# Performance work log

Measured on AMD Instinct MI355X. Metric: run time of the kernel, lower is better.

## Reference

```python
import jax, jax.numpy as jnp
import numpy as np

# Dims matching init_kwargs
B, S, D = 2, 2048, 1024
H, E, P, K = 8, 8, 128, 2
SCALE = 1.0 / np.sqrt(P)  # registered buffer 'scale'


def setup_inputs() -> dict:
    key = jax.random.key(0)
    ks = jax.random.split(key, 8)
    std = 1.0 / np.sqrt(D)  # reset_parameters uses std_scale/sqrt(input_size)
    return {
        "x": jax.random.normal(ks[0], (B, S, D), jnp.float32),
        "q_w": jax.random.normal(ks[1], (H * P, D), jnp.float32) * std,
        "k_w": jax.random.normal(ks[2], (H * P, D), jnp.float32) * std,
        "v_w": jax.random.normal(ks[3], (H * E, D, P), jnp.float32) * std,
        "o_w": jax.random.normal(ks[4], (H * E, P, D), jnp.float32) * (1.0 / np.sqrt(H * P)),
        "sel_v_w": jax.random.normal(ks[5], (H * E, D), jnp.float32) * std,
        "sel_o_w": jax.random.normal(ks[6], (H * E, D), jnp.float32) * std,
        "route_scale": jnp.ones((1,), jnp.float32),
    }


def _get_sel_gate(x, w, route_scale):
    """Faithful port of SwitchHeadCore.get_sel (eval mode, no bias):
    sigmoid routing logits per head, top-k expert selection, weight
    normalization, route_scale. Returned as a dense [B,S,H,E] gate so the
    indexed expert combine is expressed as a gated einsum (same math)."""
    logits = jnp.einsum('bsd,ed->bse', x, w).astype(jnp.float32)
    raw = logits.reshape(x.shape[0], x.shape[1], H, E)
    probs = jax.nn.sigmoid(raw)
    vals, idx = jax.lax.top_k(probs, K)                 # [B,S,H,K]
    vals = vals / jnp.clip(vals.sum(-1, keepdims=True), 1e-9)  # normalize_weights
    vals = vals * route_scale
    gate = (jax.nn.one_hot(idx, E, dtype=vals.dtype) * vals[..., None]).sum(-2)
    return gate  # [B,S,H,E]


def reference(x, q_w, k_w, v_w, o_w, sel_v_w, sel_o_w, route_scale):
    rs = route_scale[0]
    gate_v = _get_sel_gate(x, sel_v_w, rs)  # [B,S,H,E]
    gate_o = _get_sel_gate(x, sel_o_w, rs)  # [B,S,H,E]

    # q/k projections -> torch head order [B,H,S,P]
    q = jnp.einsum('bsd,hpd->bhsp', x, q_w.reshape(H, P, D))
    k = jnp.einsum('bsd,hpd->bhsp', x, k_w.reshape(H, P, D))

    # Per-token expert V projection: mixture of selected expert weight slices
    xv = jnp.einsum('bsd,hedp->bshep', x, v_w.reshape(H, E, D, P))
    v = jnp.einsum('bshep,bshe->bhsp', xv, gate_v)

    # Scaled dot-product attention (eval: no dropout)
    att = jax.nn.softmax(jnp.einsum('bhqp,bhkp->bhqk', q, k) * SCALE, axis=-1)
    ctx = jnp.einsum('bhqk,bhkp->bqhp', att, v)  # [B,S,H,P]

    # Per-token expert O projection, gated, summed over heads
    weighted = ctx[:, :, :, None, :] * gate_o[..., None]  # [B,S,H,E,P]
    out = jnp.einsum('bshep,hepd->bsd', weighted, o_w.reshape(H, E, P, D))
    return out
```

## Files before the change

### kernel.cpp

```cpp
#include <hip/hip_runtime.h>


typedef unsigned short u16;
typedef __attribute__((ext_vector_type(8))) short s8v;
typedef __attribute__((ext_vector_type(4))) float f4v;
typedef __attribute__((ext_vector_type(4))) unsigned short us4;

#define ATT_SCALE 0.08838834764831845f

__device__ inline u16 bf16_rne(float f) {
  union { float f; unsigned u; } v; v.f = f;
  unsigned r = v.u + 0x7fffu + ((v.u >> 16) & 1u);
  return (u16)(r >> 16);
}
__device__ inline float bf2f(u16 h) {
  union { unsigned u; float f; } v; v.u = ((unsigned)h) << 16;
  return v.f;
}

__device__ inline void glds16(const void* g, void* l) {
  __builtin_amdgcn_global_load_lds((const __attribute__((address_space(1))) void*)g,
                                   (__attribute__((address_space(3))) void*)l, 16, 0, 0);
}
__device__ inline int swzcol(int idx) {
  int r = idx >> 2;
  return (((idx & 3) ^ ((r + (r >> 2)) & 3)) << 3);
}
#define WAITB() do { asm volatile("s_waitcnt vmcnt(0)" ::: "memory"); __syncthreads(); } while (0)

__global__ void conv_qk(const float* __restrict__ Q, const float* __restrict__ K,
                        u16* __restrict__ Qb, u16* __restrict__ Kb) {
  int i = blockIdx.x * 256 + threadIdx.x;
  const float* src; u16* dst; int off;
  if (i < 262144) { src = Q; dst = Qb; off = i; }
  else            { src = K; dst = Kb; off = i - 262144; }
  float4 v = *(const float4*)&src[(size_t)off * 4];
  us4 o; o[0]=bf16_rne(v.x); o[1]=bf16_rne(v.y); o[2]=bf16_rne(v.z); o[3]=bf16_rne(v.w);
  *(us4*)&dst[(size_t)off * 4] = o;
}

__global__ void transpose_w(const float* __restrict__ src, u16* __restrict__ dst, int mode) {
  __shared__ float tile[32][33];
  int he = blockIdx.z;
  int C = mode ? 1024 : 128;
  int r0 = blockIdx.y * 32, c0 = blockIdx.x * 32;
  int lc = threadIdx.x & 31, rr = threadIdx.x >> 5;
  const float* s = src + (size_t)he * 131072;
#pragma unroll
  for (int i = 0; i < 4; ++i) {
    int r = rr + i * 8;
    tile[r][lc] = s[(size_t)(r0 + r) * C + c0 + lc];
  }
  __syncthreads();
#pragma unroll
  for (int i = 0; i < 4; ++i) {
    int c = rr + i * 8;
    float v = tile[lc][c];
    size_t a;
    if (mode) a = (size_t)(c0 + c) * 8192 + (size_t)he * 128 + (r0 + lc);
    else      a = (size_t)(he >> 3) * 1048576 + (size_t)(c0 + c) * 8192 + (size_t)(he & 7) * 1024 + (r0 + lc);
    dst[a] = bf16_rne(v);
  }
}

__global__ __launch_bounds__(256, 2) void routing(
    const float* __restrict__ X, const float* __restrict__ SelV, const float* __restrict__ SelO,
    const float* __restrict__ RS, int2* __restrict__ Tvi, float2* __restrict__ Tvg,
    int2* __restrict__ Toi, float2* __restrict__ Tog, u16* __restrict__ Xb) {
  __shared__ float xs[8][1024];
  __shared__ float lgs[8][128];
  int t0 = blockIdx.x * 8;
  int tid = threadIdx.x;
  for (int i = tid; i < 2048; i += 256) {
    int row = i >> 8, c = (i & 255) * 4;
    float4 v = *(const float4*)&X[(size_t)(t0 + row) * 1024 + c];
    *(float4*)&xs[row][c] = v;
    us4 o; o[0]=bf16_rne(v.x); o[1]=bf16_rne(v.y); o[2]=bf16_rne(v.z); o[3]=bf16_rne(v.w);
    *(us4*)&Xb[(size_t)(t0 + row) * 1024 + c] = o;
  }
  __syncthreads();
  {
    int widx = tid & 127, tg = tid >> 7;
    const float* w = (widx < 64) ? (SelV + (size_t)widx * 1024) : (SelO + (size_t)(widx - 64) * 1024);
    float acc[4] = {0.f, 0.f, 0.f, 0.f};
    for (int k = 0; k < 1024; k += 4) {
      float4 wv = *(const float4*)&w[k];
#pragma unroll
      for (int t = 0; t < 4; ++t) {
        float4 xv = *(const float4*)&xs[tg * 4 + t][k];
        acc[t] += wv.x * xv.x + wv.y * xv.y + wv.z * xv.z + wv.w * xv.w;
      }
    }
#pragma unroll
    for (int t = 0; t < 4; ++t) lgs[tg * 4 + t][widx] = acc[t];
  }
  __syncthreads();
  if (tid < 128) {
    float rs = RS[0];
    int tok = tid >> 4, which = (tid >> 3) & 1, h = tid & 7;
    float p[8];
#pragma unroll
    for (int e = 0; e < 8; ++e)
      p[e] = 1.f / (1.f + __expf(-lgs[tok][which * 64 + h * 8 + e]));
    float v1 = -1.f; int i1 = -1;
#pragma unroll
    for (int e = 0; e < 8; ++e) if (p[e] > v1) { v1 = p[e]; i1 = e; }
    float v2 = -1.f; int i2 = -1;
#pragma unroll
    for (int e = 0; e < 8; ++e) if (e != i1 && p[e] > v2) { v2 = p[e]; i2 = e; }
    float ssum = fmaxf(v1 + v2, 1e-9f);
    float g1 = v1 / ssum * rs, g2 = v2 / ssum * rs;
    int t = t0 + tok;
    int lo, hi; float glo, ghi;
    if (i1 < i2) { lo = i1; hi = i2; glo = g1; ghi = g2; }
    else         { lo = i2; hi = i1; glo = g2; ghi = g1; }
    if (which) { Toi[t * 8 + h] = make_int2(lo, hi); Tog[t * 8 + h] = make_float2(glo, ghi); }
    else       { Tvi[t * 8 + h] = make_int2(lo, hi); Tvg[t * 8 + h] = make_float2(glo, ghi); }
  }
}

__global__ __launch_bounds__(256) void build_buckets2(
    const int2* __restrict__ Tvi, const float2* __restrict__ Tvg,
    int* __restrict__ bcnt, u16* __restrict__ btok, float* __restrict__ bgate) {
  const int h = blockIdx.x;
  const int tid = threadIdx.x;
  const int lane = tid & 63;
  __shared__ int cnt[8];
  if (tid < 8) cnt[tid] = 0;
  __syncthreads();
  for (int chunk = 0; chunk < 16; ++chunk) {
    int t = chunk * 256 + tid;
    int2 e = Tvi[t * 8 + h];
    float2 g = Tvg[t * 8 + h];
#pragma unroll
    for (int role = 0; role < 2; ++role) {
      int mye = role ? e.y : e.x;
      float myg = role ? g.y : g.x;
      u16 entry = role ? (u16)(t | 0x8000) : (u16)t;
#pragma unroll
      for (int ee = 0; ee < 8; ++ee) {
        unsigned long long mask = __ballot(mye == ee);
        if (mye == ee) {
          int prefix = __popcll(mask & ((1ull << lane) - 1ull));
          int leader = __ffsll((unsigned long long)mask) - 1;
          int base = 0;
          if (lane == leader) base = atomicAdd(&cnt[ee], (int)__popcll(mask));
          base = __shfl(base, leader);
          int pos = base + prefix;
          btok[(h * 8 + ee) * 4096 + pos] = entry;
          bgate[(h * 8 + ee) * 4096 + pos] = myg;
        }
      }
    }
  }
  __syncthreads();
  if (tid < 8) bcnt[h * 8 + tid] = cnt[tid];
}

__global__ __launch_bounds__(256) void gemm_qk(
    const u16* __restrict__ Xb, const u16* __restrict__ Wq, const u16* __restrict__ Wk,
    u16* __restrict__ Qo, u16* __restrict__ Ko) {
  __shared__ u16 Ash0[64 * 32], Ash1[64 * 32];
  __shared__ u16 Bsh0[128 * 32], Bsh1[128 * 32];
  const int tb = blockIdx.x, nb = blockIdx.y;
  const u16* W = blockIdx.z ? Wk : Wq;
  u16* Out = blockIdx.z ? Ko : Qo;
  const int tid = threadIdx.x;
  const int wave = tid >> 6, lane = tid & 63;
  const int lg = lane >> 4, lr = lane & 15;
  const int r0 = tid >> 2, r1 = (tid + 256) >> 2;
  const int c0 = swzcol(tid), c1 = swzcol(tid + 256);
  const size_t aw  = (size_t)(tb * 64 + r0) * 1024 + c0;
  const size_t bw0 = (size_t)(nb * 128 + r0) * 1024 + c0;
  const size_t bw1 = (size_t)(nb * 128 + r1) * 1024 + c1;
  const int csl = (lg ^ ((lr + (lr >> 2)) & 3)) << 3;
  f4v acc[4][2] = {};
#define STG_QK(A, B, k0) do { \
    glds16(&Xb[aw + (k0)], &A[tid * 8]); \
    glds16(&W[bw0 + (k0)], &B[tid * 8]); \
    glds16(&W[bw1 + (k0)], &B[(tid + 256) * 8]); \
  } while (0)
#define CMP_QK(A, B) do { \
    s8v af[4], bfr[2]; \
    _Pragma("unroll") for (int m = 0; m < 4; ++m) af[m] = *(const s8v*)&A[(m * 16 + lr) * 32 + csl]; \
    _Pragma("unroll") for (int n = 0; n < 2; ++n) bfr[n] = *(const s8v*)&B[(wave * 32 + n * 16 + lr) * 32 + csl]; \
    _Pragma("unroll") for (int m = 0; m < 4; ++m) \
      _Pragma("unroll") for (int n = 0; n < 2; ++n) \
        acc[m][n] = __builtin_amdgcn_mfma_f32_16x16x32_bf16(af[m], bfr[n], acc[m][n], 0, 0, 0); \
  } while (0)
  STG_QK(Ash0, Bsh0, 0);
  for (int kt = 0; kt < 32; kt += 2) {
    WAITB();
    if (kt + 1 < 32) STG_QK(Ash1, Bsh1, (kt + 1) * 32);
    CMP_QK(Ash0, Bsh0);
    WAITB();
    if (kt + 2 < 32) STG_QK(Ash0, Bsh0, (kt + 2) * 32);
    CMP_QK(Ash1, Bsh1);
  }
#undef STG_QK
#undef CMP_QK
#pragma unroll
  for (int m = 0; m < 4; ++m) {
    int tbase = tb * 64 + m * 16 + lg * 4;
    int b = tbase >> 11, s = tbase & 2047;
#pragma unroll
    for (int n = 0; n < 2; ++n) {
      int p = wave * 32 + n * 16 + lr;
      size_t base = ((size_t)(b * 8 + nb) * 2048 + s) * 128 + p;
#pragma unroll
      for (int j = 0; j < 4; ++j)
        Out[base + (size_t)j * 128] = bf16_rne(acc[m][n][j]);
    }
  }
}

__global__ __launch_bounds__(256) void gemm_v_e(
    const u16* __restrict__ Xb, const u16* __restrict__ Vw ,
    const int* __restrict__ bcnt, const u16* __restrict__ btok,
    const float* __restrict__ bgate, u16* __restrict__ VpA, u16* __restrict__ VpB) {
  const int id = blockIdx.x + 32 * blockIdx.y;
  const int xk = id & 7, j = id >> 3;
  const int bucket = 8 * xk + (j & 7);
  const int tile = j >> 3;
  const int h = bucket >> 3, e = bucket & 7;
  const int cnt = bcnt[bucket];
  if (tile * 128 >= cnt) return;
  __shared__ u16 Ash0[128 * 32], Ash1[128 * 32];
  __shared__ u16 Bsh0[128 * 32], Bsh1[128 * 32];
  __shared__ int toksh[128];
  __shared__ float gsh[128];
  const int tid = threadIdx.x;
  if (tid < 128) {
    int ar = tile * 128 + tid;
    if (ar < cnt) {
      toksh[tid] = btok[bucket * 4096 + ar];
      gsh[tid] = bgate[bucket * 4096 + ar];
    } else { toksh[tid] = 0; gsh[tid] = 0.f; }
  }
  __syncthreads();
  const int wave = tid >> 6, lane = tid & 63;
  const int wm = wave >> 1, wn = wave & 1;
  const int lg = lane >> 4, lr = lane & 15;
  const int r0 = tid >> 2, r1 = (tid + 256) >> 2;
  const int c0 = swzcol(tid), c1 = swzcol(tid + 256);
  const size_t aw0 = (size_t)(toksh[r0] & 0xFFF) * 1024 + c0;
  const size_t aw1 = (size_t)(toksh[r1] & 0xFFF) * 1024 + c1;
  const size_t bw0 = ((size_t)(h * 128 + r0) * 8 + e) * 1024 + c0;
  const size_t bw1 = ((size_t)(h * 128 + r1) * 8 + e) * 1024 + c1;
  const int csl = (lg ^ ((lr + (lr >> 2)) & 3)) << 3;
  f4v acc[4][4] = {};
#define STG_VE(A, B, k0) do { \
    glds16(&Xb[aw0 + (k0)], &A[tid * 8]); \
    glds16(&Xb[aw1 + (k0)], &A[(tid + 256) * 8]); \
    glds16(&Vw[bw0 + (k0)], &B[tid * 8]); \
    glds16(&Vw[bw1 + (k0)], &B[(tid + 256) * 8]); \
  } while (0)
#define CMP_VE(A, B) do { \
    s8v af[4], bfr[4]; \
    _Pragma("unroll") for (int m = 0; m < 4; ++m) af[m] = *(const s8v*)&A[(wm * 64 + m * 16 + lr) * 32 + csl]; \
    _Pragma("unroll") for (int n = 0; n < 4; ++n) bfr[n] = *(const s8v*)&B[(wn * 64 + n * 16 + lr) * 32 + csl]; \
    _Pragma("unroll") for (int m = 0; m < 4; ++m) \
      _Pragma("unroll") for (int n = 0; n < 4; ++n) \
        acc[m][n] = __builtin_amdgcn_mfma_f32_16x16x32_bf16(af[m], bfr[n], acc[m][n], 0, 0, 0); \
  } while (0)
  STG_VE(Ash0, Bsh0, 0);
  for (int kt = 0; kt < 32; kt += 2) {
    WAITB();
    if (kt + 1 < 32) STG_VE(Ash1, Bsh1, (kt + 1) * 32);
    CMP_VE(Ash0, Bsh0);
    WAITB();
    if (kt + 2 < 32) STG_VE(Ash0, Bsh0, (kt + 2) * 32);
    CMP_VE(Ash1, Bsh1);
  }
#undef STG_VE
#undef CMP_VE
#pragma unroll
  for (int m = 0; m < 4; ++m) {
#pragma unroll
    for (int j2 = 0; j2 < 4; ++j2) {
      int row = wm * 64 + m * 16 + lg * 4 + j2;
      int ar = tile * 128 + row;
      if (ar < cnt) {
        int entry = toksh[row];
        int tok = entry & 0xFFF;
        u16* dst = (entry & 0x8000) ? VpB : VpA;
        float g = gsh[row];
#pragma unroll
        for (int n = 0; n < 4; ++n) {
          int p = wn * 64 + n * 16 + lr;
          dst[(size_t)tok * 1024 + h * 128 + p] = bf16_rne(g * acc[m][n][j2]);
        }
      }
    }
  }
}

__global__ void vadd_transpose(const u16* __restrict__ VpA, const u16* __restrict__ VpB,
                               u16* __restrict__ VT) {
  __shared__ u16 tile[64][136];
  const int sb = blockIdx.x, bh = blockIdx.y;
  const int b = bh >> 3, h = bh & 7;
  const int tid = threadIdx.x;
#pragma unroll
  for (int it = 0; it < 4; ++it) {
    int idx = tid + it * 256;
    int r = idx >> 4, c8 = (idx & 15) << 3;
    size_t off = (size_t)(b * 2048 + sb * 64 + r) * 1024 + h * 128 + c8;
    s8v va = *(const s8v*)&VpA[off];
    s8v vb = *(const s8v*)&VpB[off];
    s8v o;
#pragma unroll
    for (int j = 0; j < 8; ++j) o[j] = (short)bf16_rne(bf2f((u16)va[j]) + bf2f((u16)vb[j]));
    *(s8v*)&tile[r][c8] = o;
  }
  __syncthreads();
#pragma unroll
  for (int it = 0; it < 8; ++it) {
    int idx = tid + it * 256;
    int p = idx >> 4, c4 = (idx & 15) << 2;
    us4 o;
#pragma unroll
    for (int j = 0; j < 4; ++j) o[j] = tile[c4 + j][p];
    *(us4*)&VT[((size_t)bh * 128 + p) * 2048 + sb * 64 + c4] = o;
  }
}

__global__ __launch_bounds__(256, 2) void attn(
    const u16* __restrict__ Q, const u16* __restrict__ K,
    const u16* __restrict__ VT, u16* __restrict__ CTX) {
  __shared__ u16 Kt[64 * 136];
  __shared__ u16 Vt[128 * 72];
  __shared__ u16 Pl[4][16 * 72];
  const int id = blockIdx.x + 32 * blockIdx.y;
  const int xk = id & 7, j = id >> 3;
  const int bh = 2 * xk + (j >> 5);
  const int qb = j & 31;
  const int tid = threadIdx.x;
  const int wave = tid >> 6, lane = tid & 63;
  const int lg = lane >> 4, lr = lane & 15;
  const size_t base = (size_t)bh * 2048 * 128;
  const int q0 = qb * 64 + wave * 16;
  s8v qf[4];
#pragma unroll
  for (int ks = 0; ks < 4; ++ks)
    qf[ks] = *(const s8v*)&Q[base + (size_t)(q0 + lr) * 128 + ks * 32 + lg * 8];
  s8v kr[4], vr[4];
#define LOADKV(kb) do { \
    _Pragma("unroll") for (int i = 0; i < 4; ++i) { \
      int idx = tid + i * 256; \
      kr[i] = *(const s8v*)&K[base + (size_t)((kb) * 64 + (idx >> 4)) * 128 + ((idx & 15) << 3)]; \
      vr[i] = *(const s8v*)&VT[base + (size_t)(idx >> 3) * 2048 + (kb) * 64 + ((idx & 7) << 3)]; \
    } } while (0)
#define WRITEKV() do { \
    _Pragma("unroll") for (int i = 0; i < 4; ++i) { \
      int idx = tid + i * 256; \
      *(s8v*)&Kt[(idx >> 4) * 136 + ((idx & 15) << 3)] = kr[i]; \
      *(s8v*)&Vt[(idx >> 3) * 72 + ((idx & 7) << 3)] = vr[i]; \
    } } while (0)
  f4v cacc[8] = {};
  float mrun = -1e30f, ssum = 0.f;
  LOADKV(0);
  for (int kb = 0; kb < 32; ++kb) {
    asm volatile("s_waitcnt vmcnt(0)" ::: "memory");
    __syncthreads();
    WRITEKV();
    __syncthreads();
    if (kb + 1 < 32) LOADKV(kb + 1);
    f4v sc[4] = {};
    __builtin_amdgcn_s_setprio(1);
#pragma unroll
    for (int ks = 0; ks < 4; ++ks) {
#pragma unroll
      for (int m = 0; m < 4; ++m) {
        s8v ak = *(const s8v*)&Kt[(m * 16 + lr) * 136 + ks * 32 + lg * 8];
        sc[m] = __builtin_amdgcn_mfma_f32_16x16x32_bf16(ak, qf[ks], sc[m], 0, 0, 0);
      }
    }
    __builtin_amdgcn_s_setprio(0);
    float tmax = -1e30f;
#pragma unroll
    for (int m = 0; m < 4; ++m)
#pragma unroll
      for (int j2 = 0; j2 < 4; ++j2) {
        float v = sc[m][j2] * ATT_SCALE;
        sc[m][j2] = v;
        tmax = fmaxf(tmax, v);
      }
    tmax = fmaxf(tmax, __shfl_xor(tmax, 16));
    tmax = fmaxf(tmax, __shfl_xor(tmax, 32));
    float mnew = fmaxf(mrun, tmax);
    float f = __expf(mrun - mnew);
    mrun = mnew;
    float psum = 0.f;
#pragma unroll
    for (int m = 0; m < 4; ++m) {
      us4 pk;
#pragma unroll
      for (int j2 = 0; j2 < 4; ++j2) {
        float pe = __expf(sc[m][j2] - mnew);
        psum += pe;
        pk[j2] = bf16_rne(pe);
      }
      *(us4*)&Pl[wave][lr * 72 + m * 16 + lg * 4] = pk;
    }
    psum += __shfl_xor(psum, 16);
    psum += __shfl_xor(psum, 32);
    ssum = ssum * f + psum;
#pragma unroll
    for (int mr = 0; mr < 8; ++mr)
#pragma unroll
      for (int j2 = 0; j2 < 4; ++j2) cacc[mr][j2] *= f;
    __builtin_amdgcn_s_setprio(1);
#pragma unroll
    for (int ks = 0; ks < 2; ++ks) {
      s8v bp = *(const s8v*)&Pl[wave][lr * 72 + ks * 32 + lg * 8];
#pragma unroll
      for (int mr = 0; mr < 8; ++mr) {
        s8v av = *(const s8v*)&Vt[(mr * 16 + lr) * 72 + ks * 32 + lg * 8];
        cacc[mr] = __builtin_amdgcn_mfma_f32_16x16x32_bf16(av, bp, cacc[mr], 0, 0, 0);
      }
    }
    __builtin_amdgcn_s_setprio(0);
  }
#undef LOADKV
#undef WRITEKV
  float rinv = 1.f / ssum;
#pragma unroll
  for (int mr = 0; mr < 8; ++mr) {
    us4 pk;
#pragma unroll
    for (int j2 = 0; j2 < 4; ++j2) pk[j2] = bf16_rne(cacc[mr][j2] * rinv);
    *(us4*)&CTX[base + (size_t)(q0 + lr) * 128 + mr * 16 + lg * 4] = pk;
  }
}

__global__ __launch_bounds__(256) void pregate(
    const u16* __restrict__ CTX, const int2* __restrict__ Toi, const float2* __restrict__ Tog,
    u16* __restrict__ CTXG) {
  const int t = blockIdx.x;
  const int tid = threadIdx.x;
  __shared__ float gsh[64];
  if (tid < 64) {
    int h = tid >> 3, e = tid & 7;
    int2 ei = Toi[t * 8 + h];
    float2 gg = Tog[t * 8 + h];
    gsh[tid] = (e == ei.x) ? gg.x : ((e == ei.y) ? gg.y : 0.f);
  }
  __syncthreads();
  const int b = t >> 11, s = t & 2047;
#pragma unroll
  for (int c = 0; c < 4; ++c) {
    int chunk = tid + c * 256;
    int he = chunk >> 4, p8 = (chunk & 15) << 3;
    int h = he >> 3;
    float g = gsh[he];
    s8v o;
    if (g != 0.f) {
      s8v v = *(const s8v*)&CTX[((size_t)(b * 8 + h) * 2048 + s) * 128 + p8];
#pragma unroll
      for (int j = 0; j < 8; ++j) o[j] = (short)bf16_rne(bf2f((u16)v[j]) * g);
    } else {
#pragma unroll
      for (int j = 0; j < 8; ++j) o[j] = 0;
    }
    *(s8v*)&CTXG[(size_t)t * 8192 + chunk * 8] = o;
  }
}

__global__ __launch_bounds__(256) void gemm_o_dense(
    const u16* __restrict__ CTXG, const u16* __restrict__ Ow ,
    float* __restrict__ OUT, float* __restrict__ OP1a, float* __restrict__ OP1b) {
  __shared__ u16 Ash0[128 * 32], Ash1[128 * 32];
  __shared__ u16 Bsh0[128 * 32], Bsh1[128 * 32];
  const int tb = blockIdx.x, db = blockIdx.y, kz = blockIdx.z;
  const int tid = threadIdx.x;
  const int wave = tid >> 6, lane = tid & 63;
  const int wm = wave >> 1, wn = wave & 1;
  const int lg = lane >> 4, lr = lane & 15;
  const size_t kbase = (size_t)kz * 4096;
  const int r0 = tid >> 2, r1 = (tid + 256) >> 2;
  const int c0 = swzcol(tid), c1 = swzcol(tid + 256);
  const size_t aw0 = (size_t)(tb * 128 + r0) * 8192 + kbase + c0;
  const size_t aw1 = (size_t)(tb * 128 + r1) * 8192 + kbase + c1;
  const size_t bw0 = (size_t)(db * 128 + r0) * 8192 + kbase + c0;
  const size_t bw1 = (size_t)(db * 128 + r1) * 8192 + kbase + c1;
  const int csl = (lg ^ ((lr + (lr >> 2)) & 3)) << 3;
  f4v acc[4][4] = {};
#define STG_O(A, B, k0) do { \
    glds16(&CTXG[aw0 + (k0)], &A[tid * 8]); \
    glds16(&CTXG[aw1 + (k0)], &A[(tid + 256) * 8]); \
    glds16(&Ow[bw0 + (k0)], &B[tid * 8]); \
    glds16(&Ow[bw1 + (k0)], &B[(tid + 256) * 8]); \
  } while (0)
#define CMP_O(A, B) do { \
    s8v af[4], bfr[4]; \
    _Pragma("unroll") for (int m = 0; m < 4; ++m) af[m] = *(const s8v*)&A[(wm * 64 + m * 16 + lr) * 32 + csl]; \
    _Pragma("unroll") for (int n = 0; n < 4; ++n) bfr[n] = *(const s8v*)&B[(wn * 64 + n * 16 + lr) * 32 + csl]; \
    _Pragma("unroll") for (int m = 0; m < 4; ++m) \
      _Pragma("unroll") for (int n = 0; n < 4; ++n) \
        acc[m][n] = __builtin_amdgcn_mfma_f32_16x16x32_bf16(af[m], bfr[n], acc[m][n], 0, 0, 0); \
  } while (0)
  STG_O(Ash0, Bsh0, 0);
  for (int kt = 0; kt < 128; kt += 2) {
    WAITB();
    if (kt + 1 < 128) STG_O(Ash1, Bsh1, (kt + 1) * 32);
    CMP_O(Ash0, Bsh0);
    WAITB();
    if (kt + 2 < 128) STG_O(Ash0, Bsh0, (kt + 2) * 32);
    CMP_O(Ash1, Bsh1);
  }
#undef STG_O
#undef CMP_O
  float* OP;
  if (kz == 0) OP = OUT;
  else OP = (tb < 16) ? OP1a : OP1b;
  const int toff = (kz == 0) ? tb * 128 : (tb & 15) * 128;
#pragma unroll
  for (int m = 0; m < 4; ++m) {
    int t = toff + wm * 64 + m * 16 + lg * 4;
#pragma unroll
    for (int n = 0; n < 4; ++n) {
      int d = db * 128 + wn * 64 + n * 16 + lr;
#pragma unroll
      for (int j2 = 0; j2 < 4; ++j2)
        OP[(size_t)(t + j2) * 1024 + d] = acc[m][n][j2];
    }
  }
}

__global__ void add_inplace(float* __restrict__ OUT, const float* __restrict__ P0,
                            const float* __restrict__ P1) {
  size_t i = ((size_t)blockIdx.x * 256 + threadIdx.x) * 4;
  const float* P = (i < 2097152) ? (P0 + i) : (P1 + (i - 2097152));
  float4 a = *(const float4*)&OUT[i];
  float4 b = *(const float4*)P;
  *(float4*)&OUT[i] = make_float4(a.x + b.x, a.y + b.y, a.z + b.z, a.w + b.w);
}

extern "C" void kernel_launch(void* const* d_in, const int* in_sizes, int n_in,
                              void* d_out, int out_size, void* d_ws, size_t ws_size,
                              hipStream_t stream) {
  const float* x     = (const float*)d_in[0];
  const float* q_w   = (const float*)d_in[1];
  const float* k_w   = (const float*)d_in[2];
  const float* v_w   = (const float*)d_in[3];
  const float* o_w   = (const float*)d_in[4];
  const float* sel_v = (const float*)d_in[5];
  const float* sel_o = (const float*)d_in[6];
  const float* rs    = (const float*)d_in[7];

  char* ws = (char*)d_ws;
  const size_t MB = 1048576;
  const size_t KB = 1024;
  u16*    xb    = (u16*)(ws);
  u16*    ctx   = (u16*)(ws);
  float*  op1a  = (float*)(ws);
  u16*    qwb   = (u16*)(ws + 8 * MB);
  u16*    kwb   = (u16*)(ws + 10 * MB);
  u16*    ctxg  = (u16*)(ws + 8 * MB);
  u16*    vwT   = (u16*)(ws + 12 * MB);
  u16*    vt    = (u16*)(ws + 12 * MB);
  u16*    vpA   = (u16*)(ws + 28 * MB);
  u16*    vpB   = (u16*)(ws + 36 * MB);
  u16*    qh    = (u16*)(ws + 49 * MB + 512 * KB);
  u16*    kh    = (u16*)(ws + 57 * MB + 512 * KB);
  int2*   tvi   = (int2*)(ws + 72 * MB);
  float2* tvg   = (float2*)(ws + 72 * MB + 256 * KB);
  int2*   toi   = (int2*)(ws + 72 * MB + 512 * KB);
  float2* tog   = (float2*)(ws + 72 * MB + 768 * KB);
  int*    bcnt2 = (int*)(ws + 73 * MB);
  u16*    btok2 = (u16*)(ws + 73 * MB + 4 * KB);
  float*  bgate2= (float*)(ws + 73 * MB + 520 * KB);
  float*  op1b  = (float*)(ws + 72 * MB);
  u16*    owT   = (u16*)(ws + 80 * MB);
  float*  outp  = (float*)d_out;

  hipLaunchKernelGGL(conv_qk, dim3(2048), dim3(256), 0, stream, q_w, k_w, qwb, kwb);
  hipLaunchKernelGGL(transpose_w, dim3(4, 32, 64), dim3(256), 0, stream, v_w, vwT, 0);
  hipLaunchKernelGGL(transpose_w, dim3(32, 4, 64), dim3(256), 0, stream, o_w, owT, 1);
  hipLaunchKernelGGL(routing, dim3(512), dim3(256), 0, stream, x, sel_v, sel_o, rs, tvi, tvg, toi, tog, xb);
  hipLaunchKernelGGL(build_buckets2, dim3(8), dim3(256), 0, stream, tvi, tvg, bcnt2, btok2, bgate2);
  hipLaunchKernelGGL(gemm_v_e, dim3(32, 64), dim3(256), 0, stream, xb, vwT, bcnt2, btok2, bgate2, vpA, vpB);
  hipLaunchKernelGGL(vadd_transpose, dim3(32, 16), dim3(256), 0, stream, vpA, vpB, vt);
  hipLaunchKernelGGL(gemm_qk, dim3(64, 8, 2), dim3(256), 0, stream, xb, qwb, kwb, qh, kh);
  hipLaunchKernelGGL(attn, dim3(32, 16), dim3(256), 0, stream, qh, kh, vt, ctx);
  hipLaunchKernelGGL(pregate, dim3(4096), dim3(256), 0, stream, ctx, toi, tog, ctxg);
  hipLaunchKernelGGL(gemm_o_dense, dim3(32, 8, 2), dim3(256), 0, stream, ctxg, owT, outp, op1a, op1b);
  hipLaunchKernelGGL(add_inplace, dim3(4096), dim3(256), 0, stream, outp, op1a, op1b);
}
```

Measured before the change: 367.5 us.

## Merge prep kernels into one launch and fuse V-expert and QK GEMMs

Folds the weight conversion, the two weight transposes and routing into a single prep_all kernel that branches on block index. It also folds the QK projection GEMM into the expert V GEMM launch, adding 1024 extra blocks. This removes several kernel launches and the gaps between them, and lets the dense QK work fill CUs left idle by sparse expert tiles that exit early. The cost is a larger shared-memory footprint for the merged kernels, which may lower occupancy for the lighter branches.

```diff
diff --git a/kernel.cpp b/kernel.cpp
--- a/kernel.cpp
+++ b/kernel.cpp
@@ -28,94 +28,101 @@
 }
 #define WAITB() do { asm volatile("s_waitcnt vmcnt(0)" ::: "memory"); __syncthreads(); } while (0)
 
-__global__ void conv_qk(const float* __restrict__ Q, const float* __restrict__ K,
-                        u16* __restrict__ Qb, u16* __restrict__ Kb) {
-  int i = blockIdx.x * 256 + threadIdx.x;
-  const float* src; u16* dst; int off;
-  if (i < 262144) { src = Q; dst = Qb; off = i; }
-  else            { src = K; dst = Kb; off = i - 262144; }
-  float4 v = *(const float4*)&src[(size_t)off * 4];
-  us4 o; o[0]=bf16_rne(v.x); o[1]=bf16_rne(v.y); o[2]=bf16_rne(v.z); o[3]=bf16_rne(v.w);
-  *(us4*)&dst[(size_t)off * 4] = o;
-}
-
-__global__ void transpose_w(const float* __restrict__ src, u16* __restrict__ dst, int mode) {
-  __shared__ float tile[32][33];
-  int he = blockIdx.z;
-  int C = mode ? 1024 : 128;
-  int r0 = blockIdx.y * 32, c0 = blockIdx.x * 32;
-  int lc = threadIdx.x & 31, rr = threadIdx.x >> 5;
-  const float* s = src + (size_t)he * 131072;
-#pragma unroll
-  for (int i = 0; i < 4; ++i) {
-    int r = rr + i * 8;
-    tile[r][lc] = s[(size_t)(r0 + r) * C + c0 + lc];
-  }
-  __syncthreads();
-#pragma unroll
-  for (int i = 0; i < 4; ++i) {
-    int c = rr + i * 8;
-    float v = tile[lc][c];
-    size_t a;
-    if (mode) a = (size_t)(c0 + c) * 8192 + (size_t)he * 128 + (r0 + lc);
-    else      a = (size_t)(he >> 3) * 1048576 + (size_t)(c0 + c) * 8192 + (size_t)(he & 7) * 1024 + (r0 + lc);
-    dst[a] = bf16_rne(v);
-  }
-}
-
-__global__ __launch_bounds__(256, 2) void routing(
+__global__ __launch_bounds__(256, 2) void prep_all(
+    const float* __restrict__ Qw, const float* __restrict__ Kw,
+    const float* __restrict__ Vw, const float* __restrict__ Ow,
     const float* __restrict__ X, const float* __restrict__ SelV, const float* __restrict__ SelO,
-    const float* __restrict__ RS, int2* __restrict__ Tvi, float2* __restrict__ Tvg,
+    const float* __restrict__ RS,
+    u16* __restrict__ Qb, u16* __restrict__ Kb, u16* __restrict__ vwT, u16* __restrict__ owT,
+    int2* __restrict__ Tvi, float2* __restrict__ Tvg,
     int2* __restrict__ Toi, float2* __restrict__ Tog, u16* __restrict__ Xb) {
-  __shared__ float xs[8][1024];
-  __shared__ float lgs[8][128];
-  int t0 = blockIdx.x * 8;
-  int tid = threadIdx.x;
-  for (int i = tid; i < 2048; i += 256) {
-    int row = i >> 8, c = (i & 255) * 4;
-    float4 v = *(const float4*)&X[(size_t)(t0 + row) * 1024 + c];
-    *(float4*)&xs[row][c] = v;
+  __shared__ __align__(16) char smem[36864];
+  const int id = blockIdx.x;
+  const int tid = threadIdx.x;
+  if (id < 2048) {
+    int i = id * 256 + tid;
+    const float* src; u16* dst; int off;
+    if (i < 262144) { src = Qw; dst = Qb; off = i; }
+    else            { src = Kw; dst = Kb; off = i - 262144; }
+    float4 v = *(const float4*)&src[(size_t)off * 4];
     us4 o; o[0]=bf16_rne(v.x); o[1]=bf16_rne(v.y); o[2]=bf16_rne(v.z); o[3]=bf16_rne(v.w);
-    *(us4*)&Xb[(size_t)(t0 + row) * 1024 + c] = o;
-  }
-  __syncthreads();
-  {
-    int widx = tid & 127, tg = tid >> 7;
-    const float* w = (widx < 64) ? (SelV + (size_t)widx * 1024) : (SelO + (size_t)(widx - 64) * 1024);
-    float acc[4] = {0.f, 0.f, 0.f, 0.f};
-    for (int k = 0; k < 1024; k += 4) {
-      float4 wv = *(const float4*)&w[k];
-#pragma unroll
-      for (int t = 0; t < 4; ++t) {
-        float4 xv = *(const float4*)&xs[tg * 4 + t][k];
-        acc[t] += wv.x * xv.x + wv.y * xv.y + wv.z * xv.z + wv.w * xv.w;
-      }
-    }
-#pragma unroll
-    for (int t = 0; t < 4; ++t) lgs[tg * 4 + t][widx] = acc[t];
-  }
-  __syncthreads();
-  if (tid < 128) {
-    float rs = RS[0];
-    int tok = tid >> 4, which = (tid >> 3) & 1, h = tid & 7;
-    float p[8];
-#pragma unroll
-    for (int e = 0; e < 8; ++e)
-      p[e] = 1.f / (1.f + __expf(-lgs[tok][which * 64 + h * 8 + e]));
-    float v1 = -1.f; int i1 = -1;
-#pragma unroll
-    for (int e = 0; e < 8; ++e) if (p[e] > v1) { v1 = p[e]; i1 = e; }
-    float v2 = -1.f; int i2 = -1;
-#pragma unroll
-    for (int e = 0; e < 8; ++e) if (e != i1 && p[e] > v2) { v2 = p[e]; i2 = e; }
-    float ssum = fmaxf(v1 + v2, 1e-9f);
-    float g1 = v1 / ssum * rs, g2 = v2 / ssum * rs;
-    int t = t0 + tok;
-    int lo, hi; float glo, ghi;
-    if (i1 < i2) { lo = i1; hi = i2; glo = g1; ghi = g2; }
-    else         { lo = i2; hi = i1; glo = g2; ghi = g1; }
-    if (which) { Toi[t * 8 + h] = make_int2(lo, hi); Tog[t * 8 + h] = make_float2(glo, ghi); }
-    else       { Tvi[t * 8 + h] = make_int2(lo, hi); Tvg[t * 8 + h] = make_float2(glo, ghi); }
+    *(us4*)&dst[(size_t)off * 4] = o;
+  } else if (id < 18432) {
+    float* tile = (float*)smem;
+    int mode, bx, by, he;
+    if (id < 10240) { int rel = id - 2048;  mode = 0; bx = rel & 3;  by = (rel >> 2) & 31; he = rel >> 7; }
+    else            { int rel = id - 10240; mode = 1; bx = rel & 31; by = (rel >> 5) & 3;  he = rel >> 7; }
+    const float* src = mode ? Ow : Vw;
+    u16* dst = mode ? owT : vwT;
+    int C = mode ? 1024 : 128;
+    int r0 = by * 32, c0 = bx * 32;
+    int lc = tid & 31, rr = tid >> 5;
+    const float* s = src + (size_t)he * 131072;
+#pragma unroll
+    for (int i = 0; i < 4; ++i) {
+      int r = rr + i * 8;
+      tile[r * 33 + lc] = s[(size_t)(r0 + r) * C + c0 + lc];
+    }
+    __syncthreads();
+#pragma unroll
+    for (int i = 0; i < 4; ++i) {
+      int c = rr + i * 8;
+      float v = tile[lc * 33 + c];
+      size_t a;
+      if (mode) a = (size_t)(c0 + c) * 8192 + (size_t)he * 128 + (r0 + lc);
+      else      a = (size_t)(he >> 3) * 1048576 + (size_t)(c0 + c) * 8192 + (size_t)(he & 7) * 1024 + (r0 + lc);
+      dst[a] = bf16_rne(v);
+    }
+  } else {
+    float* xs  = (float*)smem;
+    float* lgs = (float*)(smem + 32768);
+    int t0 = (id - 18432) * 8;
+    for (int i = tid; i < 2048; i += 256) {
+      int row = i >> 8, c = (i & 255) * 4;
+      float4 v = *(const float4*)&X[(size_t)(t0 + row) * 1024 + c];
+      *(float4*)&xs[row * 1024 + c] = v;
+      us4 o; o[0]=bf16_rne(v.x); o[1]=bf16_rne(v.y); o[2]=bf16_rne(v.z); o[3]=bf16_rne(v.w);
+      *(us4*)&Xb[(size_t)(t0 + row) * 1024 + c] = o;
+    }
+    __syncthreads();
+    {
+      int widx = tid & 127, tg = tid >> 7;
+      const float* w = (widx < 64) ? (SelV + (size_t)widx * 1024) : (SelO + (size_t)(widx - 64) * 1024);
+      float acc[4] = {0.f, 0.f, 0.f, 0.f};
+      for (int k = 0; k < 1024; k += 4) {
+        float4 wv = *(const float4*)&w[k];
+#pragma unroll
+        for (int t = 0; t < 4; ++t) {
+          float4 xv = *(const float4*)&xs[(tg * 4 + t) * 1024 + k];
+          acc[t] += wv.x * xv.x + wv.y * xv.y + wv.z * xv.z + wv.w * xv.w;
+        }
+      }
+#pragma unroll
+      for (int t = 0; t < 4; ++t) lgs[(tg * 4 + t) * 128 + widx] = acc[t];
+    }
+    __syncthreads();
+    if (tid < 128) {
+      float rs = RS[0];
+      int tok = tid >> 4, which = (tid >> 3) & 1, h = tid & 7;
+      float p[8];
+#pragma unroll
+      for (int e = 0; e < 8; ++e)
+        p[e] = 1.f / (1.f + __expf(-lgs[tok * 128 + which * 64 + h * 8 + e]));
+      float v1 = -1.f; int i1 = -1;
+#pragma unroll
+      for (int e = 0; e < 8; ++e) if (p[e] > v1) { v1 = p[e]; i1 = e; }
+      float v2 = -1.f; int i2 = -1;
+#pragma unroll
+      for (int e = 0; e < 8; ++e) if (e != i1 && p[e] > v2) { v2 = p[e]; i2 = e; }
+      float ssum = fmaxf(v1 + v2, 1e-9f);
+      float g1 = v1 / ssum * rs, g2 = v2 / ssum * rs;
+      int t = t0 + tok;
+      int lo, hi; float glo, ghi;
+      if (i1 < i2) { lo = i1; hi = i2; glo = g1; ghi = g2; }
+      else         { lo = i2; hi = i1; glo = g2; ghi = g1; }
+      if (which) { Toi[t * 8 + h] = make_int2(lo, hi); Tog[t * 8 + h] = make_float2(glo, ghi); }
+      else       { Tvi[t * 8 + h] = make_int2(lo, hi); Tvg[t * 8 + h] = make_float2(glo, ghi); }
+    }
   }
 }
 
@@ -157,98 +164,44 @@
   if (tid < 8) bcnt[h * 8 + tid] = cnt[tid];
 }
 
-__global__ __launch_bounds__(256) void gemm_qk(
-    const u16* __restrict__ Xb, const u16* __restrict__ Wq, const u16* __restrict__ Wk,
+__global__ __launch_bounds__(256) void gemm_v_qk(
+    const u16* __restrict__ Xb, const u16* __restrict__ Vw,
+    const int* __restrict__ bcnt, const u16* __restrict__ btok,
+    const float* __restrict__ bgate, u16* __restrict__ VpA, u16* __restrict__ VpB,
+    const u16* __restrict__ Wq, const u16* __restrict__ Wk,
     u16* __restrict__ Qo, u16* __restrict__ Ko) {
-  __shared__ u16 Ash0[64 * 32], Ash1[64 * 32];
+  __shared__ u16 Ash0[128 * 32], Ash1[128 * 32];
   __shared__ u16 Bsh0[128 * 32], Bsh1[128 * 32];
-  const int tb = blockIdx.x, nb = blockIdx.y;
-  const u16* W = blockIdx.z ? Wk : Wq;
-  u16* Out = blockIdx.z ? Ko : Qo;
+  __shared__ int toksh[128];
+  __shared__ float gsh[128];
   const int tid = threadIdx.x;
   const int wave = tid >> 6, lane = tid & 63;
   const int lg = lane >> 4, lr = lane & 15;
   const int r0 = tid >> 2, r1 = (tid + 256) >> 2;
   const int c0 = swzcol(tid), c1 = swzcol(tid + 256);
-  const size_t aw  = (size_t)(tb * 64 + r0) * 1024 + c0;
-  const size_t bw0 = (size_t)(nb * 128 + r0) * 1024 + c0;
-  const size_t bw1 = (size_t)(nb * 128 + r1) * 1024 + c1;
   const int csl = (lg ^ ((lr + (lr >> 2)) & 3)) << 3;
-  f4v acc[4][2] = {};
-#define STG_QK(A, B, k0) do { \
-    glds16(&Xb[aw + (k0)], &A[tid * 8]); \
-    glds16(&W[bw0 + (k0)], &B[tid * 8]); \
-    glds16(&W[bw1 + (k0)], &B[(tid + 256) * 8]); \
-  } while (0)
-#define CMP_QK(A, B) do { \
-    s8v af[4], bfr[2]; \
-    _Pragma("unroll") for (int m = 0; m < 4; ++m) af[m] = *(const s8v*)&A[(m * 16 + lr) * 32 + csl]; \
-    _Pragma("unroll") for (int n = 0; n < 2; ++n) bfr[n] = *(const s8v*)&B[(wave * 32 + n * 16 + lr) * 32 + csl]; \
-    _Pragma("unroll") for (int m = 0; m < 4; ++m) \
-      _Pragma("unroll") for (int n = 0; n < 2; ++n) \
-        acc[m][n] = __builtin_amdgcn_mfma_f32_16x16x32_bf16(af[m], bfr[n], acc[m][n], 0, 0, 0); \
-  } while (0)
-  STG_QK(Ash0, Bsh0, 0);
-  for (int kt = 0; kt < 32; kt += 2) {
-    WAITB();
-    if (kt + 1 < 32) STG_QK(Ash1, Bsh1, (kt + 1) * 32);
-    CMP_QK(Ash0, Bsh0);
-    WAITB();
-    if (kt + 2 < 32) STG_QK(Ash0, Bsh0, (kt + 2) * 32);
-    CMP_QK(Ash1, Bsh1);
-  }
-#undef STG_QK
-#undef CMP_QK
-#pragma unroll
-  for (int m = 0; m < 4; ++m) {
-    int tbase = tb * 64 + m * 16 + lg * 4;
-    int b = tbase >> 11, s = tbase & 2047;
-#pragma unroll
-    for (int n = 0; n < 2; ++n) {
-      int p = wave * 32 + n * 16 + lr;
-      size_t base = ((size_t)(b * 8 + nb) * 2048 + s) * 128 + p;
-#pragma unroll
-      for (int j = 0; j < 4; ++j)
-        Out[base + (size_t)j * 128] = bf16_rne(acc[m][n][j]);
-    }
-  }
-}
-
-__global__ __launch_bounds__(256) void gemm_v_e(
-    const u16* __restrict__ Xb, const u16* __restrict__ Vw ,
-    const int* __restrict__ bcnt, const u16* __restrict__ btok,
-    const float* __restrict__ bgate, u16* __restrict__ VpA, u16* __restrict__ VpB) {
-  const int id = blockIdx.x + 32 * blockIdx.y;
-  const int xk = id & 7, j = id >> 3;
-  const int bucket = 8 * xk + (j & 7);
-  const int tile = j >> 3;
-  const int h = bucket >> 3, e = bucket & 7;
-  const int cnt = bcnt[bucket];
-  if (tile * 128 >= cnt) return;
-  __shared__ u16 Ash0[128 * 32], Ash1[128 * 32];
-  __shared__ u16 Bsh0[128 * 32], Bsh1[128 * 32];
-  __shared__ int toksh[128];
-  __shared__ float gsh[128];
-  const int tid = threadIdx.x;
-  if (tid < 128) {
-    int ar = tile * 128 + tid;
-    if (ar < cnt) {
-      toksh[tid] = btok[bucket * 4096 + ar];
-      gsh[tid] = bgate[bucket * 4096 + ar];
-    } else { toksh[tid] = 0; gsh[tid] = 0.f; }
-  }
-  __syncthreads();
-  const int wave = tid >> 6, lane = tid & 63;
-  const int wm = wave >> 1, wn = wave & 1;
-  const int lg = lane >> 4, lr = lane & 15;
-  const int r0 = tid >> 2, r1 = (tid + 256) >> 2;
-  const int c0 = swzcol(tid), c1 = swzcol(tid + 256);
-  const size_t aw0 = (size_t)(toksh[r0] & 0xFFF) * 1024 + c0;
-  const size_t aw1 = (size_t)(toksh[r1] & 0xFFF) * 1024 + c1;
-  const size_t bw0 = ((size_t)(h * 128 + r0) * 8 + e) * 1024 + c0;
-  const size_t bw1 = ((size_t)(h * 128 + r1) * 8 + e) * 1024 + c1;
-  const int csl = (lg ^ ((lr + (lr >> 2)) & 3)) << 3;
-  f4v acc[4][4] = {};
+  if (blockIdx.y < 64) {
+    const int id = blockIdx.x + 32 * blockIdx.y;
+    const int xk = id & 7, j = id >> 3;
+    const int bucket = 8 * xk + (j & 7);
+    const int tile = j >> 3;
+    const int h = bucket >> 3, e = bucket & 7;
+    const int cnt = bcnt[bucket];
+    if (tile * 128 >= cnt) return;
+    if (tid < 128) {
+      int ar = tile * 128 + tid;
+      if (ar < cnt) {
+        toksh[tid] = btok[bucket * 4096 + ar];
+        gsh[tid] = bgate[bucket * 4096 + ar];
+      } else { toksh[tid] = 0; gsh[tid] = 0.f; }
+    }
+    __syncthreads();
+    const int wm = wave >> 1, wn = wave & 1;
+    const size_t aw0 = (size_t)(toksh[r0] & 0xFFF) * 1024 + c0;
+    const size_t aw1 = (size_t)(toksh[r1] & 0xFFF) * 1024 + c1;
+    const size_t bw0 = ((size_t)(h * 128 + r0) * 8 + e) * 1024 + c0;
+    const size_t bw1 = ((size_t)(h * 128 + r1) * 8 + e) * 1024 + c1;
+    f4v acc[4][4] = {};
 #define STG_VE(A, B, k0) do { \
     glds16(&Xb[aw0 + (k0)], &A[tid * 8]); \
     glds16(&Xb[aw1 + (k0)], &A[(tid + 256) * 8]); \
@@ -263,33 +216,80 @@
       _Pragma("unroll") for (int n = 0; n < 4; ++n) \
         acc[m][n] = __builtin_amdgcn_mfma_f32_16x16x32_bf16(af[m], bfr[n], acc[m][n], 0, 0, 0); \
   } while (0)
-  STG_VE(Ash0, Bsh0, 0);
-  for (int kt = 0; kt < 32; kt += 2) {
-    WAITB();
-    if (kt + 1 < 32) STG_VE(Ash1, Bsh1, (kt + 1) * 32);
-    CMP_VE(Ash0, Bsh0);
-    WAITB();
-    if (kt + 2 < 32) STG_VE(Ash0, Bsh0, (kt + 2) * 32);
-    CMP_VE(Ash1, Bsh1);
-  }
+    STG_VE(Ash0, Bsh0, 0);
+    for (int kt = 0; kt < 32; kt += 2) {
+      WAITB();
+      if (kt + 1 < 32) STG_VE(Ash1, Bsh1, (kt + 1) * 32);
+      CMP_VE(Ash0, Bsh0);
+      WAITB();
+      if (kt + 2 < 32) STG_VE(Ash0, Bsh0, (kt + 2) * 32);
+      CMP_VE(Ash1, Bsh1);
+    }
 #undef STG_VE
 #undef CMP_VE
 #pragma unroll
-  for (int m = 0; m < 4; ++m) {
-#pragma unroll
-    for (int j2 = 0; j2 < 4; ++j2) {
-      int row = wm * 64 + m * 16 + lg * 4 + j2;
-      int ar = tile * 128 + row;
-      if (ar < cnt) {
-        int entry = toksh[row];
-        int tok = entry & 0xFFF;
-        u16* dst = (entry & 0x8000) ? VpB : VpA;
-        float g = gsh[row];
-#pragma unroll
-        for (int n = 0; n < 4; ++n) {
-          int p = wn * 64 + n * 16 + lr;
-          dst[(size_t)tok * 1024 + h * 128 + p] = bf16_rne(g * acc[m][n][j2]);
+    for (int m = 0; m < 4; ++m) {
+#pragma unroll
+      for (int j2 = 0; j2 < 4; ++j2) {
+        int row = wm * 64 + m * 16 + lg * 4 + j2;
+        int ar = tile * 128 + row;
+        if (ar < cnt) {
+          int entry = toksh[row];
+          int tok = entry & 0xFFF;
+          u16* dst = (entry & 0x8000) ? VpB : VpA;
+          float g = gsh[row];
+#pragma unroll
+          for (int n = 0; n < 4; ++n) {
+            int p = wn * 64 + n * 16 + lr;
+            dst[(size_t)tok * 1024 + h * 128 + p] = bf16_rne(g * acc[m][n][j2]);
+          }
         }
+      }
+    }
+  } else {
+    const int qid = blockIdx.x + 32 * (blockIdx.y - 64);
+    const int tb = qid & 63, nb = (qid >> 6) & 7, z = qid >> 9;
+    const u16* W = z ? Wk : Wq;
+    u16* Out = z ? Ko : Qo;
+    const size_t aw  = (size_t)(tb * 64 + r0) * 1024 + c0;
+    const size_t bw0 = (size_t)(nb * 128 + r0) * 1024 + c0;
+    const size_t bw1 = (size_t)(nb * 128 + r1) * 1024 + c1;
+    f4v acc[4][2] = {};
+#define STG_QK(A, B, k0) do { \
+    glds16(&Xb[aw + (k0)], &A[tid * 8]); \
+    glds16(&W[bw0 + (k0)], &B[tid * 8]); \
+    glds16(&W[bw1 + (k0)], &B[(tid + 256) * 8]); \
+  } while (0)
+#define CMP_QK(A, B) do { \
+    s8v af[4], bfr[2]; \
+    _Pragma("unroll") for (int m = 0; m < 4; ++m) af[m] = *(const s8v*)&A[(m * 16 + lr) * 32 + csl]; \
+    _Pragma("unroll") for (int n = 0; n < 2; ++n) bfr[n] = *(const s8v*)&B[(wave * 32 + n * 16 + lr) * 32 + csl]; \
+    _Pragma("unroll") for (int m = 0; m < 4; ++m) \
+      _Pragma("unroll") for (int n = 0; n < 2; ++n) \
+        acc[m][n] = __builtin_amdgcn_mfma_f32_16x16x32_bf16(af[m], bfr[n], acc[m][n], 0, 0, 0); \
+  } while (0)
+    STG_QK(Ash0, Bsh0, 0);
+    for (int kt = 0; kt < 32; kt += 2) {
+      WAITB();
+      if (kt + 1 < 32) STG_QK(Ash1, Bsh1, (kt + 1) * 32);
+      CMP_QK(Ash0, Bsh0);
+      WAITB();
+      if (kt + 2 < 32) STG_QK(Ash0, Bsh0, (kt + 2) * 32);
+      CMP_QK(Ash1, Bsh1);
+    }
+#undef STG_QK
+#undef CMP_QK
+#pragma unroll
+    for (int m = 0; m < 4; ++m) {
+      int tbase = tb * 64 + m * 16 + lg * 4;
+      int b = tbase >> 11, s = tbase & 2047;
+#pragma unroll
+      for (int n = 0; n < 2; ++n) {
+        int p = wave * 32 + n * 16 + lr;
+        size_t base = ((size_t)(b * 8 + nb) * 2048 + s) * 128 + p;
+#pragma unroll
+        for (int j2 = 0; j2 < 4; ++j2)
+          Out[base + (size_t)j2 * 128] = bf16_rne(acc[m][n][j2]);
       }
     }
   }
@@ -468,7 +468,7 @@
 }
 
 __global__ __launch_bounds__(256) void gemm_o_dense(
-    const u16* __restrict__ CTXG, const u16* __restrict__ Ow ,
+    const u16* __restrict__ CTXG, const u16* __restrict__ Ow,
     float* __restrict__ OUT, float* __restrict__ OP1a, float* __restrict__ OP1b) {
   __shared__ u16 Ash0[128 * 32], Ash1[128 * 32];
   __shared__ u16 Bsh0[128 * 32], Bsh1[128 * 32];
@@ -575,14 +575,13 @@
   u16*    owT   = (u16*)(ws + 80 * MB);
   float*  outp  = (float*)d_out;
 
-  hipLaunchKernelGGL(conv_qk, dim3(2048), dim3(256), 0, stream, q_w, k_w, qwb, kwb);
-  hipLaunchKernelGGL(transpose_w, dim3(4, 32, 64), dim3(256), 0, stream, v_w, vwT, 0);
-  hipLaunchKernelGGL(transpose_w, dim3(32, 4, 64), dim3(256), 0, stream, o_w, owT, 1);
-  hipLaunchKernelGGL(routing, dim3(512), dim3(256), 0, stream, x, sel_v, sel_o, rs, tvi, tvg, toi, tog, xb);
+  hipLaunchKernelGGL(prep_all, dim3(18944), dim3(256), 0, stream,
+                     q_w, k_w, v_w, o_w, x, sel_v, sel_o, rs,
+                     qwb, kwb, vwT, owT, tvi, tvg, toi, tog, xb);
   hipLaunchKernelGGL(build_buckets2, dim3(8), dim3(256), 0, stream, tvi, tvg, bcnt2, btok2, bgate2);
-  hipLaunchKernelGGL(gemm_v_e, dim3(32, 64), dim3(256), 0, stream, xb, vwT, bcnt2, btok2, bgate2, vpA, vpB);
+  hipLaunchKernelGGL(gemm_v_qk, dim3(32, 96), dim3(256), 0, stream,
+                     xb, vwT, bcnt2, btok2, bgate2, vpA, vpB, qwb, kwb, qh, kh);
   hipLaunchKernelGGL(vadd_transpose, dim3(32, 16), dim3(256), 0, stream, vpA, vpB, vt);
-  hipLaunchKernelGGL(gemm_qk, dim3(64, 8, 2), dim3(256), 0, stream, xb, qwb, kwb, qh, kh);
   hipLaunchKernelGGL(attn, dim3(32, 16), dim3(256), 0, stream, qh, kh, vt, ctx);
   hipLaunchKernelGGL(pregate, dim3(4096), dim3(256), 0, stream, ctx, toi, tog, ctxg);
   hipLaunchKernelGGL(gemm_o_dense, dim3(32, 8, 2), dim3(256), 0, stream, ctxg, owT, outp, op1a, op1b);
```

New measurement: 418.6 us. 1.14x slower.
